# Kernel tuning notes

Measured on AMD Instinct MI355X. Metric: run time of the kernel, lower is better.

The kernel has to match this reference:

```python
import jax, jax.numpy as jnp
import numpy as np
from jax import lax

B, C, H, W = 4, 256, 32, 32   # latent: NCHW, C == codebook embed dim
N_CODES = 16384


def setup_inputs() -> dict:
    key = jax.random.key(0)
    k1, k2, k3 = jax.random.split(key, 3)
    latent = jax.random.normal(k1, (B, C, H, W), jnp.float32)
    codebook = jax.random.normal(k2, (N_CODES, C), jnp.float32)
    dec_w = jax.random.normal(k3, (3, C, 3, 3), jnp.float32) * 0.02
    dec_b = jnp.zeros((3,), jnp.float32)
    return {"latent": latent, "codebook": codebook, "dec_w": dec_w, "dec_b": dec_b}


def vector_quantize(x, codebook):
    # x: [B,H,W,D], codebook: [N,D]. Squared-L2 nearest neighbor + gather,
    # straight-through gradient (replace_grad(x_q, x)).
    d = ((x * x).sum(-1, keepdims=True)
         - 2.0 * jnp.einsum('bhwd,nd->bhwn', x, codebook)
         + (codebook * codebook).sum(-1))          # [B,H,W,N]
    idx = jnp.argmin(d, axis=-1)                    # [B,H,W]
    x_q = codebook[idx]                             # gather -> [B,H,W,D]
    return x + lax.stop_gradient(x_q - x)


@jax.custom_vjp
def clamp_with_grad(x):
    return jnp.clip(x, 0.0, 1.0)

def _cwg_fwd(x):
    return jnp.clip(x, 0.0, 1.0), x

def _cwg_bwd(x, g):
    # pass gradient only where it points back toward the valid range
    keep = (g * (x - jnp.clip(x, 0.0, 1.0)) >= 0).astype(g.dtype)
    return (g * keep,)

clamp_with_grad.defvjp(_cwg_fwd, _cwg_bwd)


def decode(quant, dec_w, dec_b):
    # stub VQGAN decoder: single 3x3 conv embed_dim -> 3 (NCHW)
    y = lax.conv_general_dilated(quant, dec_w, window_strides=(1, 1),
                                 padding='SAME',
                                 dimension_numbers=('NCHW', 'OIHW', 'NCHW'))
    return y + dec_b[None, :, None, None]


def reference(latent, codebook, dec_w, dec_b):
    x = jnp.moveaxis(latent, 1, 3)                  # NCHW -> NHWC
    quant = jnp.moveaxis(vector_quantize(x, codebook), 3, 1)  # back to NCHW
    img = decode(quant, dec_w, dec_b)
    return clamp_with_grad((img + 1.0) * 0.5)
```

## Files before the change

kernel.cpp:

```cpp
#include <hip/hip_runtime.h>
#include <hip/hip_bf16.h>
#include <stdint.h>

#define P_TOT   4096
#define N_CODE  16384
#define DIM     256
#define HW      1024
#define CHW     262144
#define NBLK    16

typedef unsigned long long u64;
typedef unsigned short u16;
typedef __attribute__((ext_vector_type(4))) float f32x4;
typedef __attribute__((ext_vector_type(8))) short bf16x8;
typedef __attribute__((ext_vector_type(8))) unsigned short ushort8;

#define FENCE() asm volatile("" ::: "memory")
#define BAR()   __builtin_amdgcn_s_barrier()
#define VM(n)   asm volatile("s_waitcnt vmcnt(" #n ")" ::: "memory")

__device__ __forceinline__ unsigned int mono(float f) {
  unsigned int u = __float_as_uint(f);
  return (u & 0x80000000u) ? ~u : (u | 0x80000000u);
}
__device__ __forceinline__ u16 f2bf(float f) {
  __hip_bfloat16 h = __float2bfloat16(f);
  return *(u16*)&h;
}
__device__ __forceinline__ float bf2f(u16 b) {
  __hip_bfloat16 h = *(__hip_bfloat16*)&b;
  return __bfloat162float(h);
}
__device__ __forceinline__ void gload16(const void* g, void* l) {
  __builtin_amdgcn_global_load_lds(
      (const __attribute__((address_space(1))) unsigned int*)g,
      (__attribute__((address_space(3))) unsigned int*)l, 16, 0, 0);
}

__global__ __launch_bounds__(256) void k_prep(const float* __restrict__ cb,
                                              const float* __restrict__ latent,
                                              const float* __restrict__ dec_w,
                                              u16* __restrict__ bfrag,
                                              u16* __restrict__ xfrag,
                                              float* __restrict__ cnorm,
                                              float* __restrict__ wt) {
  __shared__ float ls[64][68];
  int bid = blockIdx.x;
  int t = threadIdx.x;
  if (bid < 1024) {
    int blk = bid;
    int kp = blk & 3, bq = (blk >> 2) & 3, nb = blk >> 4;
    int code0 = nb * 256 + bq * 64;
    int k0 = kp * 64;
    int lr = t >> 4, lc = (t & 15) * 4;
    #pragma unroll
    for (int pss = 0; pss < 4; ++pss) {
      int row = pss * 16 + lr;
      float4 v = *(const float4*)&cb[(size_t)(code0 + row) * DIM + k0 + lc];
      ls[row][lc] = v.x; ls[row][lc + 1] = v.y; ls[row][lc + 2] = v.z; ls[row][lc + 3] = v.w;
    }
    __syncthreads();
    int row64 = t & 63, g = t >> 6;
    #pragma unroll
    for (int it = 0; it < 4; ++it) {
      int combo = it * 4 + g;
      int kt2 = combo >> 3, s = (combo >> 1) & 3, h = combo & 1;
      int kt = kp * 2 + kt2;
      ushort8 o;
      #pragma unroll
      for (int e = 0; e < 8; ++e) {
        float x = ls[row64][kt2 * 32 + s * 8 + e];
        u16 hi = f2bf(x);
        o[e] = h ? f2bf(x - bf2f(hi)) : hi;
      }
      size_t unitIdx = (size_t)(nb * 8 + kt) * 4 + bq;
      *(ushort8*)&bfrag[unitIdx * 4096 + (size_t)((h * 4 + s) * 64 + row64) * 8] = o;
    }
  } else if (bid < 1280) {
    int blk = bid - 1024;
    int kp = blk & 3, rowblk = blk >> 2;
    int g0 = rowblk * 64;
    int b = g0 >> 10, hw0 = g0 & 1023;
    int c0 = kp * 64;
    int ch = t >> 4, px4 = (t & 15) * 4;
    #pragma unroll
    for (int pss = 0; pss < 4; ++pss) {
      int c = pss * 16 + ch;
      float4 v = *(const float4*)&latent[(size_t)b * CHW + (size_t)(c0 + c) * HW + hw0 + px4];
      ls[px4 + 0][c] = v.x; ls[px4 + 1][c] = v.y; ls[px4 + 2][c] = v.z; ls[px4 + 3][c] = v.w;
    }
    __syncthreads();
    int row64 = t & 63, g = t >> 6;
    #pragma unroll
    for (int it = 0; it < 4; ++it) {
      int combo = it * 4 + g;
      int kt2 = combo >> 3, s = (combo >> 1) & 3, h = combo & 1;
      int kt = kp * 2 + kt2;
      ushort8 o;
      #pragma unroll
      for (int e = 0; e < 8; ++e) {
        float x = ls[row64][kt2 * 32 + s * 8 + e];
        u16 hi = f2bf(x);
        o[e] = h ? f2bf(x - bf2f(hi)) : hi;
      }
      int mbO = rowblk >> 2, aq = rowblk & 3;
      size_t unitIdx = (size_t)(mbO * 8 + kt) * 4 + aq;
      *(ushort8*)&xfrag[unitIdx * 4096 + (size_t)((h * 4 + s) * 64 + row64) * 8] = o;
    }
  } else if (bid < 5376) {
    int code = (bid - 1280) * 4 + (t >> 6);
    int lane = t & 63;
    float4 v = ((const float4*)(cb + (size_t)code * DIM))[lane];
    float sv = fmaf(v.x, v.x, fmaf(v.y, v.y, fmaf(v.z, v.z, v.w * v.w)));
    #pragma unroll
    for (int off = 32; off; off >>= 1) sv += __shfl_down(sv, off, 64);
    if (lane == 0) cnorm[code] = sv;
  } else {
    int e = (bid - 5376) * 256 + t;
    if (e < 6912) {
      int ic = e & 255; int r = e >> 8;
      int kx = r % 3; r /= 3; int ky = r % 3; int oc = r / 3;
      wt[e] = dec_w[((oc * 256 + ic) * 3 + ky) * 3 + kx];
    }
  }
}

__global__ __launch_bounds__(512, 2) void k_vq(const u16* __restrict__ xfrag,
                                               const u16* __restrict__ bfrag,
                                               const float* __restrict__ cnorm,
                                               u64* __restrict__ partial) {
  __shared__ u16 lds[2][2][4][4096];
  __shared__ float cnl[1024];

  int bid = blockIdx.x;
  int xcd = bid & 7, ix = bid >> 3;
  int nbc = xcd * 2 + (ix >> 4);
  int mb  = ix & 15;

  int tid = threadIdx.x, lane = tid & 63, w = tid >> 6;
  int fr = lane & 15, s = lane >> 4;
  int aq = w >> 1;
  int rbase = (w & 1) * 32;
  int tid8 = tid * 8;

  const u16* Xb = xfrag + (size_t)mb * 32 * 4096;
  const u16* Bb = bfrag + (size_t)nbc * 128 * 4096;

  cnl[tid]       = cnorm[nbc * 1024 + tid];
  cnl[tid + 512] = cnorm[nbc * 1024 + 512 + tid];
  __syncthreads();

  #pragma unroll
  for (int r = 0; r < 4; ++r) gload16(Xb + (size_t)r * 4096 + tid8, &lds[0][0][r][0] + tid8);
  gload16(Bb + (size_t)0 * 4096 + tid8, &lds[0][1][0][0] + tid8);
  gload16(Bb + (size_t)1 * 4096 + tid8, &lds[0][1][1][0] + tid8);
  gload16(Bb + (size_t)2 * 4096 + tid8, &lds[0][1][2][0] + tid8);
  gload16(Bb + (size_t)3 * 4096 + tid8, &lds[0][1][3][0] + tid8);
  VM(2); BAR(); FENCE();

  f32x4 acc[2][16] = {};
  u64 best[4]  = {~0ull, ~0ull, ~0ull, ~0ull};
  u64 best2[4] = {~0ull, ~0ull, ~0ull, ~0ull};
  bf16x8 ah[2], al[2], bh[4], bl[4];

  #define READ_A(LA)                                                          \
    _Pragma("unroll")                                                         \
    for (int m = 0; m < 2; ++m) {                                             \
      ah[m] = *(const bf16x8*)&(LA)[aq * 4096 + (size_t)((0 + s) * 64 + rbase + m * 16 + fr) * 8]; \
      al[m] = *(const bf16x8*)&(LA)[aq * 4096 + (size_t)((4 + s) * 64 + rbase + m * 16 + fr) * 8]; \
    }
  #define READ_B(LB, q)                                                       \
    _Pragma("unroll")                                                         \
    for (int j = 0; j < 4; ++j) {                                             \
      bh[j] = *(const bf16x8*)&(LB)[(q) * 4096 + (size_t)((0 + s) * 64 + j * 16 + fr) * 8]; \
      bl[j] = *(const bf16x8*)&(LB)[(q) * 4096 + (size_t)((4 + s) * 64 + j * 16 + fr) * 8]; \
    }
  #define MFMAQ(q)                                                            \
    __builtin_amdgcn_s_setprio(1);                                            \
    _Pragma("unroll")                                                         \
    for (int m = 0; m < 2; ++m) {                                             \
      _Pragma("unroll")                                                       \
      for (int j = 0; j < 4; ++j)                                             \
        acc[m][(q) * 4 + j] = __builtin_amdgcn_mfma_f32_16x16x32_bf16(ah[m], bh[j], acc[m][(q) * 4 + j], 0, 0, 0); \
    }                                                                         \
    _Pragma("unroll")                                                         \
    for (int m = 0; m < 2; ++m) {                                             \
      _Pragma("unroll")                                                       \
      for (int j = 0; j < 4; ++j)                                             \
        acc[m][(q) * 4 + j] = __builtin_amdgcn_mfma_f32_16x16x32_bf16(ah[m], bl[j], acc[m][(q) * 4 + j], 0, 0, 0); \
    }                                                                         \
    _Pragma("unroll")                                                         \
    for (int m = 0; m < 2; ++m) {                                             \
      _Pragma("unroll")                                                       \
      for (int j = 0; j < 4; ++j)                                             \
        acc[m][(q) * 4 + j] = __builtin_amdgcn_mfma_f32_16x16x32_bf16(al[m], bh[j], acc[m][(q) * 4 + j], 0, 0, 0); \
    }                                                                         \
    __builtin_amdgcn_s_setprio(0);
  #define FOLD(pp)                                                            \
    _Pragma("unroll")                                                         \
    for (int n = 0; n < 16; ++n) {                                            \
      float cnv = cnl[(pp) * 256 + n * 16 + fr];                              \
      unsigned code = (unsigned)(nbc * 1024 + (pp) * 256 + n * 16 + fr);      \
      _Pragma("unroll")                                                       \
      for (int r = 0; r < 4; ++r) {                                           \
        float v0 = fmaf(-2.0f, acc[0][n][r], cnv);                            \
        u64 k0 = ((u64)mono(v0) << 32) | code;                                \
        if (k0 < best[r]) best[r] = k0;                                       \
        acc[0][n][r] = 0.0f;                                                  \
        float v1 = fmaf(-2.0f, acc[1][n][r], cnv);                            \
        u64 k1 = ((u64)mono(v1) << 32) | code;                                \
        if (k1 < best2[r]) best2[r] = k1;                                     \
        acc[1][n][r] = 0.0f;                                                  \
      }                                                                       \
    }

  #pragma unroll 1
  for (int tt = 0; tt < 32; ++tt) {
    const int cur = tt & 1, nxt = cur ^ 1;
    const int kt = tt & 7;
    u16* LA = &lds[cur][0][0][0];
    u16* LB = &lds[cur][1][0][0];
    const u16* SA = Xb + (size_t)((tt + 1) & 7) * 16384;
    const u16* SB = Bb + (size_t)(tt + 1) * 16384;
    const bool stage = (tt < 31);
    READ_A(LA); READ_B(LB, 0);
    if (stage) {
      #pragma unroll
      for (int r = 0; r < 4; ++r) gload16(SA + (size_t)r * 4096 + tid8, &lds[nxt][0][r][0] + tid8);
      gload16(SB + (size_t)0 * 4096 + tid8, &lds[nxt][1][0][0] + tid8);
      gload16(SB + (size_t)1 * 4096 + tid8, &lds[nxt][1][1][0] + tid8);
    }
    BAR();
    MFMAQ(0);
    READ_B(LB, 1);
    MFMAQ(1);
    if (stage) { VM(6); } else { VM(0); }
    BAR(); FENCE();
    READ_B(LB, 2);
    if (stage) {
      gload16(SB + (size_t)2 * 4096 + tid8, &lds[nxt][1][2][0] + tid8);
      gload16(SB + (size_t)3 * 4096 + tid8, &lds[nxt][1][3][0] + tid8);
    }
    BAR();
    MFMAQ(2);
    READ_B(LB, 3);
    MFMAQ(3);
    if (kt == 7) { FOLD(tt >> 3); }
    if (stage) { VM(2); }
    BAR(); FENCE();
  }

  #pragma unroll
  for (int d = 1; d < 16; d <<= 1) {
    #pragma unroll
    for (int r = 0; r < 4; ++r) {
      u64 o = __shfl_xor(best[r], d, 64);
      if (o < best[r]) best[r] = o;
      u64 o2 = __shfl_xor(best2[r], d, 64);
      if (o2 < best2[r]) best2[r] = o2;
    }
  }
  if (fr == 0) {
    int rowb = mb * 256 + w * 32 + s * 4;
    #pragma unroll
    for (int r = 0; r < 4; ++r) {
      partial[(size_t)(rowb + r) * NBLK + nbc] = best[r];
      partial[(size_t)(rowb + 16 + r) * NBLK + nbc] = best2[r];
    }
  }
}

__global__ __launch_bounds__(256) void k_conv(const u64* __restrict__ partial,
                                              const float* __restrict__ latent,
                                              const float* __restrict__ cb,
                                              const float* __restrict__ wt,
                                              const float* __restrict__ bias,
                                              float* __restrict__ out) {
  __shared__ int idxl[3][32];
  int y = blockIdx.x, b = blockIdx.y;
  int t = threadIdx.x;
  int px = t >> 3, sub = t & 7;
  #pragma unroll 1
  for (int r = 0; r < 3; ++r) {
    int yy = min(max(y + r - 1, 0), 31);
    int p = b * HW + yy * 32 + px;
    u64 v0 = partial[(size_t)p * NBLK + sub];
    u64 v1 = partial[(size_t)p * NBLK + 8 + sub];
    u64 m1 = v0 < v1 ? v0 : v1;
    #pragma unroll
    for (int d = 1; d < 8; d <<= 1) { u64 o = __shfl_xor(m1, d, 64); if (o < m1) m1 = o; }
    u64 w0 = (v0 == m1) ? ~0ull : v0;
    u64 w1 = (v1 == m1) ? ~0ull : v1;
    u64 m2 = w0 < w1 ? w0 : w1;
    #pragma unroll
    for (int d = 1; d < 8; d <<= 1) { u64 o = __shfl_xor(m2, d, 64); if (o < m2) m2 = o; }
    int n1 = (int)(m1 & 0xFFFFFFFFull);
    int n2 = (int)(m2 & 0xFFFFFFFFull);
    const float* xb = latent + (size_t)b * CHW + yy * 32 + px;
    double d1 = 0.0, d2 = 0.0;
    #pragma unroll
    for (int q = 0; q < 32; ++q) {
      int c = sub * 32 + q;
      double xv = (double)xb[(size_t)c * HW];
      double e1 = xv - (double)cb[(size_t)n1 * DIM + c]; d1 += e1 * e1;
      double e2 = xv - (double)cb[(size_t)n2 * DIM + c]; d2 += e2 * e2;
    }
    #pragma unroll
    for (int d = 1; d < 8; d <<= 1) { d1 += __shfl_xor(d1, d, 64); d2 += __shfl_xor(d2, d, 64); }
    if (sub == 0) idxl[r][px] = (d2 < d1 || (d2 == d1 && n2 < n1)) ? n2 : n1;
  }
  __syncthreads();

  int x = t & 31, icg = t >> 5;
  float a0 = 0.f, a1 = 0.f, a2 = 0.f;
  #pragma unroll
  for (int dy = -1; dy <= 1; dy++) {
    int yy = y + dy;
    if (yy < 0 || yy >= 32) continue;
    #pragma unroll
    for (int dx = -1; dx <= 1; dx++) {
      int xx = x + dx;
      if (xx < 0 || xx >= 32) continue;
      int n = idxl[dy + 1][xx];
      const float4* crow = (const float4*)(cb + (size_t)n * DIM + icg * 32);
      int tap = (dy + 1) * 3 + (dx + 1);
      const float4* w0p = (const float4*)(wt + (size_t)(0 * 9 + tap) * DIM + icg * 32);
      const float4* w1p = (const float4*)(wt + (size_t)(1 * 9 + tap) * DIM + icg * 32);
      const float4* w2p = (const float4*)(wt + (size_t)(2 * 9 + tap) * DIM + icg * 32);
      #pragma unroll
      for (int q = 0; q < 8; q++) {
        float4 qv = crow[q];
        float4 wa = w0p[q];
        a0 = fmaf(qv.x, wa.x, a0); a0 = fmaf(qv.y, wa.y, a0);
        a0 = fmaf(qv.z, wa.z, a0); a0 = fmaf(qv.w, wa.w, a0);
        float4 wb = w1p[q];
        a1 = fmaf(qv.x, wb.x, a1); a1 = fmaf(qv.y, wb.y, a1);
        a1 = fmaf(qv.z, wb.z, a1); a1 = fmaf(qv.w, wb.w, a1);
        float4 wcv = w2p[q];
        a2 = fmaf(qv.x, wcv.x, a2); a2 = fmaf(qv.y, wcv.y, a2);
        a2 = fmaf(qv.z, wcv.z, a2); a2 = fmaf(qv.w, wcv.w, a2);
      }
    }
  }
  __shared__ float red[3][32][8];
  red[0][x][icg] = a0; red[1][x][icg] = a1; red[2][x][icg] = a2;
  __syncthreads();
  if (t < 96) {
    int oc = t >> 5, xo = t & 31;
    float sum = 0.f;
    #pragma unroll
    for (int k = 0; k < 8; k++) sum += red[oc][xo][k];
    sum += bias[oc];
    sum = (sum + 1.0f) * 0.5f;
    sum = fminf(fmaxf(sum, 0.0f), 1.0f);
    out[((size_t)(b * 3 + oc) * 32 + y) * 32 + xo] = sum;
  }
}

extern "C" void kernel_launch(void* const* d_in, const int* in_sizes, int n_in,
                              void* d_out, int out_size, void* d_ws, size_t ws_size,
                              hipStream_t stream) {
  const float* latent = (const float*)d_in[0];
  const float* cb     = (const float*)d_in[1];
  const float* dec_w  = (const float*)d_in[2];
  const float* dec_b  = (const float*)d_in[3];
  float* out = (float*)d_out;

  char* ws = (char*)d_ws;
  u64*   partial = (u64*)ws;
  float* cnorm   = (float*)(ws + 0x080000);
  float* wt      = (float*)(ws + 0x094000);
  u16*   xfrag   = (u16*)  (ws + 0x100000);
  u16*   bfrag   = (u16*)  (ws + 0x800000);

  k_prep<<<dim3(5403), dim3(256), 0, stream>>>(cb, latent, dec_w, bfrag, xfrag, cnorm, wt);
  k_vq  <<<dim3(256),  dim3(512), 0, stream>>>(xfrag, bfrag, cnorm, partial);
  k_conv<<<dim3(32, 4), dim3(256), 0, stream>>>(partial, latent, cb, wt, dec_b, out);
}
```

Before: 216.9 us.

## Split index refinement into separate kernel and simplify VQ loop staging

Moves the top-2 candidate merge and double-precision distance check out of the conv kernel into a dedicated k_idx kernel. It uses one wavefront per pixel, so each pixel is processed once instead of roughly three times across neighbouring rows. The VQ GEMM loop is also restructured to issue all next-stage B loads at once, drop the intermediate barriers, and wait for all loads at the end of each iteration. This reduces redundant work and raises parallelism, but adds a kernel launch and may lose load/compute overlap in the main loop.

```diff
diff --git a/kernel.cpp b/kernel.cpp
--- a/kernel.cpp
+++ b/kernel.cpp
@@ -152,11 +152,9 @@
 
   #pragma unroll
   for (int r = 0; r < 4; ++r) gload16(Xb + (size_t)r * 4096 + tid8, &lds[0][0][r][0] + tid8);
-  gload16(Bb + (size_t)0 * 4096 + tid8, &lds[0][1][0][0] + tid8);
-  gload16(Bb + (size_t)1 * 4096 + tid8, &lds[0][1][1][0] + tid8);
-  gload16(Bb + (size_t)2 * 4096 + tid8, &lds[0][1][2][0] + tid8);
-  gload16(Bb + (size_t)3 * 4096 + tid8, &lds[0][1][3][0] + tid8);
-  VM(2); BAR(); FENCE();
+  #pragma unroll
+  for (int r = 0; r < 4; ++r) gload16(Bb + (size_t)r * 4096 + tid8, &lds[0][1][r][0] + tid8);
+  VM(0); BAR(); FENCE();
 
   f32x4 acc[2][16] = {};
   u64 best[4]  = {~0ull, ~0ull, ~0ull, ~0ull};
@@ -227,26 +225,18 @@
     if (stage) {
       #pragma unroll
       for (int r = 0; r < 4; ++r) gload16(SA + (size_t)r * 4096 + tid8, &lds[nxt][0][r][0] + tid8);
-      gload16(SB + (size_t)0 * 4096 + tid8, &lds[nxt][1][0][0] + tid8);
-      gload16(SB + (size_t)1 * 4096 + tid8, &lds[nxt][1][1][0] + tid8);
-    }
-    BAR();
+      #pragma unroll
+      for (int r = 0; r < 4; ++r) gload16(SB + (size_t)r * 4096 + tid8, &lds[nxt][1][r][0] + tid8);
+    }
     MFMAQ(0);
     READ_B(LB, 1);
     MFMAQ(1);
-    if (stage) { VM(6); } else { VM(0); }
-    BAR(); FENCE();
     READ_B(LB, 2);
-    if (stage) {
-      gload16(SB + (size_t)2 * 4096 + tid8, &lds[nxt][1][2][0] + tid8);
-      gload16(SB + (size_t)3 * 4096 + tid8, &lds[nxt][1][3][0] + tid8);
-    }
-    BAR();
     MFMAQ(2);
     READ_B(LB, 3);
     MFMAQ(3);
     if (kt == 7) { FOLD(tt >> 3); }
-    if (stage) { VM(2); }
+    VM(0);
     BAR(); FENCE();
   }
 
@@ -270,8 +260,44 @@
   }
 }
 
-__global__ __launch_bounds__(256) void k_conv(const u64* __restrict__ partial,
-                                              const float* __restrict__ latent,
+__global__ __launch_bounds__(256) void k_idx(const u64* __restrict__ partial,
+                                             const float* __restrict__ latent,
+                                             const float* __restrict__ cb,
+                                             int* __restrict__ idxo) {
+  int p = (blockIdx.x * 256 + threadIdx.x) >> 6;
+  int lane = threadIdx.x & 63;
+  u64 v = (lane < NBLK) ? partial[(size_t)p * NBLK + lane] : ~0ull;
+  u64 m1 = v;
+  #pragma unroll
+  for (int d = 1; d < 64; d <<= 1) { u64 o = __shfl_xor(m1, d, 64); if (o < m1) m1 = o; }
+  u64 vv = (v == m1) ? ~0ull : v;
+  u64 m2 = vv;
+  #pragma unroll
+  for (int d = 1; d < 64; d <<= 1) { u64 o = __shfl_xor(m2, d, 64); if (o < m2) m2 = o; }
+  int n1 = (int)(m1 & 0xFFFFFFFFull);
+  int n2 = (int)(m2 & 0xFFFFFFFFull);
+
+  int b = p >> 10, hw = p & 1023;
+  const float* xb = latent + (size_t)b * CHW + hw;
+  double d1 = 0.0, d2 = 0.0;
+  #pragma unroll
+  for (int q = 0; q < 4; ++q) {
+    int c = lane * 4 + q;
+    double xv = (double)xb[(size_t)c * HW];
+    double e1 = xv - (double)cb[(size_t)n1 * DIM + c]; d1 += e1 * e1;
+    double e2 = xv - (double)cb[(size_t)n2 * DIM + c]; d2 += e2 * e2;
+  }
+  #pragma unroll
+  for (int d = 32; d; d >>= 1) {
+    d1 += __shfl_down(d1, d, 64);
+    d2 += __shfl_down(d2, d, 64);
+  }
+  if (lane == 0) {
+    idxo[p] = (d2 < d1 || (d2 == d1 && n2 < n1)) ? n2 : n1;
+  }
+}
+
+__global__ __launch_bounds__(256) void k_conv(const int* __restrict__ idxo,
                                               const float* __restrict__ cb,
                                               const float* __restrict__ wt,
                                               const float* __restrict__ bias,
@@ -279,35 +305,10 @@
   __shared__ int idxl[3][32];
   int y = blockIdx.x, b = blockIdx.y;
   int t = threadIdx.x;
-  int px = t >> 3, sub = t & 7;
-  #pragma unroll 1
-  for (int r = 0; r < 3; ++r) {
+  if (t < 96) {
+    int r = t >> 5, px = t & 31;
     int yy = min(max(y + r - 1, 0), 31);
-    int p = b * HW + yy * 32 + px;
-    u64 v0 = partial[(size_t)p * NBLK + sub];
-    u64 v1 = partial[(size_t)p * NBLK + 8 + sub];
-    u64 m1 = v0 < v1 ? v0 : v1;
-    #pragma unroll
-    for (int d = 1; d < 8; d <<= 1) { u64 o = __shfl_xor(m1, d, 64); if (o < m1) m1 = o; }
-    u64 w0 = (v0 == m1) ? ~0ull : v0;
-    u64 w1 = (v1 == m1) ? ~0ull : v1;
-    u64 m2 = w0 < w1 ? w0 : w1;
-    #pragma unroll
-    for (int d = 1; d < 8; d <<= 1) { u64 o = __shfl_xor(m2, d, 64); if (o < m2) m2 = o; }
-    int n1 = (int)(m1 & 0xFFFFFFFFull);
-    int n2 = (int)(m2 & 0xFFFFFFFFull);
-    const float* xb = latent + (size_t)b * CHW + yy * 32 + px;
-    double d1 = 0.0, d2 = 0.0;
-    #pragma unroll
-    for (int q = 0; q < 32; ++q) {
-      int c = sub * 32 + q;
-      double xv = (double)xb[(size_t)c * HW];
-      double e1 = xv - (double)cb[(size_t)n1 * DIM + c]; d1 += e1 * e1;
-      double e2 = xv - (double)cb[(size_t)n2 * DIM + c]; d2 += e2 * e2;
-    }
-    #pragma unroll
-    for (int d = 1; d < 8; d <<= 1) { d1 += __shfl_xor(d1, d, 64); d2 += __shfl_xor(d2, d, 64); }
-    if (sub == 0) idxl[r][px] = (d2 < d1 || (d2 == d1 && n2 < n1)) ? n2 : n1;
+    idxl[r][px] = idxo[b * HW + yy * 32 + px];
   }
   __syncthreads();
 
@@ -369,11 +370,13 @@
   char* ws = (char*)d_ws;
   u64*   partial = (u64*)ws;
   float* cnorm   = (float*)(ws + 0x080000);
+  int*   idx     = (int*)  (ws + 0x090000);
   float* wt      = (float*)(ws + 0x094000);
   u16*   xfrag   = (u16*)  (ws + 0x100000);
   u16*   bfrag   = (u16*)  (ws + 0x800000);
 
   k_prep<<<dim3(5403), dim3(256), 0, stream>>>(cb, latent, dec_w, bfrag, xfrag, cnorm, wt);
   k_vq  <<<dim3(256),  dim3(512), 0, stream>>>(xfrag, bfrag, cnorm, partial);
-  k_conv<<<dim3(32, 4), dim3(256), 0, stream>>>(partial, latent, cb, wt, dec_b, out);
-}
+  k_idx <<<dim3(1024), dim3(256), 0, stream>>>(partial, latent, cb, idx);
+  k_conv<<<dim3(32, 4), dim3(256), 0, stream>>>(idx, cb, wt, dec_b, out);
+}
```

Measured after the change: 191.7 us. 1.13x faster.
